# Kernel tuning notes

Measured on AMD Instinct MI355X. Metric: run time of the kernel, lower is better.

Reference implementation:

```python
import jax, jax.numpy as jnp
import numpy as np

B, N, H, E = 1, 50000, 8, 32
P = 1_600_000  # num edges


def setup_inputs() -> dict:
    key = jax.random.key(0)
    kq, kk, kv, ka = jax.random.split(key, 4)
    queries = jax.random.normal(kq, (B, N, H, E), dtype=jnp.float32)
    keys = jax.random.normal(kk, (B, N, H, E), dtype=jnp.float32)
    values = jax.random.normal(kv, (B, N, H, E), dtype=jnp.float32)
    adj = jax.random.randint(ka, (2, P), 0, N, dtype=jnp.int32)
    return {"queries": queries, "keys": keys, "values": values, "adj": adj}


def reference(queries, keys, values, adj):
    # queries/keys: (B, N, H, E); values: (B, N, H, D); adj: (2, P) COO edges
    b, n, h, e = queries.shape
    temp = 1.0 / np.sqrt(e).astype(np.float32)
    src, dst = adj[0], adj[1]
    # per-edge scaled dot product: (P, B, H), edge axis leading for segment ops
    s = temp * jnp.einsum("bphe,bphe->pbh", queries[:, src], keys[:, dst])
    # segment (scatter) softmax keyed by target node src
    m = jax.ops.segment_max(s, src, num_segments=n)          # (N, B, H)
    p = jnp.exp(s - m[src])                                   # (P, B, H)
    den = jax.ops.segment_sum(p, src, num_segments=n)        # (N, B, H)
    alpha = p / den[src]                                      # (P, B, H)
    # sparse weighted aggregation (spmm): out[i] = sum_{e: src==i} alpha_e * v[dst_e]
    vg = jnp.moveaxis(values[:, dst], 0, 1)                   # (P, B, H, D)
    out = jax.ops.segment_sum(alpha[..., None] * vg, src, num_segments=n)  # (N, B, H, D)
    return jnp.moveaxis(out, 0, 1)                            # (B, N, H, D)
```

## Files before the change

### kernel.cpp

```cpp
#include <hip/hip_runtime.h>
#include <hip/hip_fp16.h>
#include <math.h>

#define HEADS 8
#define EDIM 32
#define ROW (HEADS * EDIM)

typedef _Float16 h2_t __attribute__((ext_vector_type(2)));

__device__ __forceinline__ void pack_one(const float* __restrict__ k, const float* __restrict__ v,
                                         uint4* __restrict__ kvh, long t) {
    const float4 kf = *reinterpret_cast<const float4*>(k + t * 4);
    const float4 vf = *reinterpret_cast<const float4*>(v + t * 4);
    __half2 h0 = __floats2half2_rn(kf.x, kf.y);
    __half2 h1 = __floats2half2_rn(kf.z, kf.w);
    __half2 h2 = __floats2half2_rn(vf.x, vf.y);
    __half2 h3 = __floats2half2_rn(vf.z, vf.w);
    uint4 o;
    o.x = *reinterpret_cast<unsigned int*>(&h0);
    o.y = *reinterpret_cast<unsigned int*>(&h1);
    o.z = *reinterpret_cast<unsigned int*>(&h2);
    o.w = *reinterpret_cast<unsigned int*>(&h3);
    kvh[t] = o;
}

__global__ __launch_bounds__(256) void prep_fused_kernel(
    const float* __restrict__ k, const float* __restrict__ v, uint4* __restrict__ kvh,
    const int* __restrict__ src, const int* __restrict__ dst,
    int* __restrict__ counts, int* __restrict__ padded,
    int N, int P, int scatBlocks, int cap, int copies)
{
    if ((int)blockIdx.x < scatBlocks) {
        const int copy = (int)blockIdx.x & (copies - 1);
        int* __restrict__ cnt = counts + (size_t)copy * N;
        int* __restrict__ pad = padded + (size_t)copy * N * cap;
        const int P2 = P >> 1;
        const int stride = scatBlocks * 256;
        int i = (int)blockIdx.x * 256 + threadIdx.x;
        for (; i < P2; i += stride) {
            const int2 s2 = reinterpret_cast<const int2*>(src)[i];
            const int2 d2 = reinterpret_cast<const int2*>(dst)[i];
            int pos = atomicAdd(&cnt[s2.x], 1);
            if (pos < cap) pad[(size_t)s2.x * cap + pos] = d2.x;
            pos = atomicAdd(&cnt[s2.y], 1);
            if (pos < cap) pad[(size_t)s2.y * cap + pos] = d2.y;
        }
        if ((P & 1) && blockIdx.x == 0 && threadIdx.x == 0) {
            const int s = src[P - 1];
            const int pos = atomicAdd(&cnt[s], 1);
            if (pos < cap) pad[(size_t)s * cap + pos] = dst[P - 1];
        }
    } else {
        const long t = (long)((int)blockIdx.x - scatBlocks) * 256 + threadIdx.x;
        if (t < (long)N * 64) pack_one(k, v, kvh, t);
    }
}

__global__ __launch_bounds__(256) void pack_kernel(const float* __restrict__ k,
                                                   const float* __restrict__ v,
                                                   uint4* __restrict__ kvh, long total) {
    const long t = (long)blockIdx.x * blockDim.x + threadIdx.x;
    if (t < total) pack_one(k, v, kvh, t);
}

__global__ void hist_kernel(const int* __restrict__ src, int* __restrict__ counts, int P) {
    int i = blockIdx.x * blockDim.x + threadIdx.x;
    int stride = gridDim.x * blockDim.x;
    for (; i < P; i += stride) atomicAdd(&counts[src[i]], 1);
}

__global__ __launch_bounds__(1024) void scan_block(const int* __restrict__ counts,
                                                   int* __restrict__ loc_excl,
                                                   int* __restrict__ bsums, int n) {
    __shared__ int wsum[16];
    const int lane = threadIdx.x & 63;
    const int wv = threadIdx.x >> 6;
    const int i = blockIdx.x * 1024 + threadIdx.x;
    const int val = (i < n) ? counts[i] : 0;
    int incl = val;
    #pragma unroll
    for (int off = 1; off < 64; off <<= 1) {
        int t = __shfl_up(incl, off);
        if (lane >= off) incl += t;
    }
    if (lane == 63) wsum[wv] = incl;
    __syncthreads();
    if (threadIdx.x < 16) {
        int wval = wsum[threadIdx.x];
        int winc = wval;
        #pragma unroll
        for (int off = 1; off < 16; off <<= 1) {
            int t = __shfl_up(winc, off);
            if ((int)threadIdx.x >= off) winc += t;
        }
        wsum[threadIdx.x] = winc - wval;
    }
    __syncthreads();
    const int ex = wsum[wv] + incl - val;
    if (i < n) loc_excl[i] = ex;
    if (threadIdx.x == 1023) bsums[blockIdx.x] = ex + val;
}

__global__ void scan_tops(const int* __restrict__ bsums, int* __restrict__ bbase,
                          int nb, int* __restrict__ total_out) {
    const int lane = threadIdx.x & 63;
    int base = 0;
    for (int start = 0; start < nb; start += 64) {
        const int idx = start + lane;
        const int v = (idx < nb) ? bsums[idx] : 0;
        int incl = v;
        #pragma unroll
        for (int off = 1; off < 64; off <<= 1) {
            int t = __shfl_up(incl, off);
            if (lane >= off) incl += t;
        }
        if (idx < nb) bbase[idx] = base + incl - v;
        base += __shfl(incl, 63);
    }
    if (lane == 0) *total_out = base;
}

__global__ void scan_add(const int* __restrict__ loc_excl, const int* __restrict__ bbase,
                         int* __restrict__ offsets, int* __restrict__ cursors, int n) {
    const int i = blockIdx.x * blockDim.x + threadIdx.x;
    if (i < n) {
        const int o = loc_excl[i] + bbase[i >> 10];
        offsets[i] = o;
        cursors[i] = o;
    }
}

__global__ void scatter_kernel(const int* __restrict__ src, const int* __restrict__ dst,
                               int* __restrict__ cursors, int* __restrict__ sorted_dst, int P) {
    int i = blockIdx.x * blockDim.x + threadIdx.x;
    int stride = gridDim.x * blockDim.x;
    for (; i < P; i += stride) {
        int s = src[i];
        int pos = atomicAdd(&cursors[s], 1);
        sorted_dst[pos] = dst[i];
    }
}

__device__ __forceinline__ void edge_accum(const uint4 raw, const h2_t qh01, const h2_t qh23,
                                           float& lsum, float4& acc) {
    const h2_t k01 = *reinterpret_cast<const h2_t*>(&raw.x);
    const h2_t k23 = *reinterpret_cast<const h2_t*>(&raw.y);
    const float2 v01 = __half22float2(*reinterpret_cast<const __half2*>(&raw.z));
    const float2 v23 = __half22float2(*reinterpret_cast<const __half2*>(&raw.w));
    float p = __builtin_amdgcn_fdot2(qh01, k01,
              __builtin_amdgcn_fdot2(qh23, k23, 0.0f, false), false);
    p += __shfl_xor(p, 1);
    p += __shfl_xor(p, 2);
    p += __shfl_xor(p, 4);
    const float w = __expf(p);
    lsum += w;
    acc.x += w * v01.x; acc.y += w * v01.y;
    acc.z += w * v23.x; acc.w += w * v23.y;
}

__global__ __launch_bounds__(256) void attn_kernel_h(
    const float* __restrict__ q, const uint4* __restrict__ kv,
    const int* __restrict__ counts_or_offsets, const int* __restrict__ edges,
    float* __restrict__ out, int N, float temp, int cap, int copies)
{
    const int wave = threadIdx.x >> 6;
    const int lane = threadIdx.x & 63;
    const int node = blockIdx.x * 4 + wave;
    if (node >= N) return;

    float4 qv = *reinterpret_cast<const float4*>(q + (size_t)node * ROW + lane * 4);
    qv.x *= temp; qv.y *= temp; qv.z *= temp; qv.w *= temp;
    const __half2 qp01 = __floats2half2_rn(qv.x, qv.y);
    const __half2 qp23 = __floats2half2_rn(qv.z, qv.w);
    const h2_t qh01 = *reinterpret_cast<const h2_t*>(&qp01);
    const h2_t qh23 = *reinterpret_cast<const h2_t*>(&qp23);
    const uint4* kvl = kv + lane;

    float lsum = 0.0f;
    float4 acc = {0.f, 0.f, 0.f, 0.f};

    if (cap > 0) {
        for (int c = 0; c < copies; ++c) {
            int cnt = counts_or_offsets[(size_t)c * N + node];
            cnt = (cnt < cap) ? cnt : cap;
            const int* __restrict__ bucket = edges + ((size_t)c * N + node) * cap;
            int i = 0;
            for (; i + 2 <= cnt; i += 2) {
                const int d0 = bucket[i];
                const int d1 = bucket[i + 1];
                const uint4 r0 = kvl[(size_t)d0 * 64];
                const uint4 r1 = kvl[(size_t)d1 * 64];
                edge_accum(r0, qh01, qh23, lsum, acc);
                edge_accum(r1, qh01, qh23, lsum, acc);
            }
            if (i < cnt) {
                const uint4 r = kvl[(size_t)bucket[i] * 64];
                edge_accum(r, qh01, qh23, lsum, acc);
            }
        }
    } else {
        int e = counts_or_offsets[node];
        const int end = counts_or_offsets[node + 1];
        for (; e + 2 <= end; e += 2) {
            const int d0 = edges[e];
            const int d1 = edges[e + 1];
            const uint4 r0 = kvl[(size_t)d0 * 64];
            const uint4 r1 = kvl[(size_t)d1 * 64];
            edge_accum(r0, qh01, qh23, lsum, acc);
            edge_accum(r1, qh01, qh23, lsum, acc);
        }
        if (e < end) {
            const uint4 r = kvl[(size_t)edges[e] * 64];
            edge_accum(r, qh01, qh23, lsum, acc);
        }
    }

    const float inv = (lsum > 0.0f) ? (1.0f / lsum) : 0.0f;
    float4 o;
    o.x = acc.x * inv; o.y = acc.y * inv; o.z = acc.z * inv; o.w = acc.w * inv;
    *reinterpret_cast<float4*>(out + (size_t)node * ROW + lane * 4) = o;
}

extern "C" void kernel_launch(void* const* d_in, const int* in_sizes, int n_in,
                              void* d_out, int out_size, void* d_ws, size_t ws_size,
                              hipStream_t stream) {
    const float* q = (const float*)d_in[0];
    const float* k = (const float*)d_in[1];
    const float* v = (const float*)d_in[2];
    const int*   adj = (const int*)d_in[3];

    const int N = in_sizes[0] / ROW;
    const int P = in_sizes[3] / 2;
    const int* src = adj;
    const int* dst = adj + P;

    const float temp = 1.0f / sqrtf((float)EDIM);
    const size_t kv_bytes = (size_t)N * 64 * sizeof(uint4);

    const int tier_copies[3] = {8, 4, 1};
    const int tier_cap[3]    = {20, 28, 96};

    for (int t = 0; t < 3; ++t) {
        const int copies = tier_copies[t];
        const int cap = tier_cap[t];
        const size_t int_bytes = (size_t)copies * N * (1 + cap) * sizeof(int);
        const size_t kv_off = (int_bytes + 15) & ~(size_t)15;
        if (ws_size < kv_off + kv_bytes) continue;

        int* counts = (int*)d_ws;
        int* padded = counts + (size_t)copies * N;
        uint4* kvh = (uint4*)((char*)d_ws + kv_off);

        hipMemsetAsync(counts, 0, (size_t)copies * N * sizeof(int), stream);

        const int packBlocks = (int)(((long)N * 64 + 255) / 256);
        const int scatBlocks = 3072;
        prep_fused_kernel<<<scatBlocks + packBlocks, 256, 0, stream>>>(
            k, v, kvh, src, dst, counts, padded, N, P, scatBlocks, cap, copies);

        attn_kernel_h<<<(N + 3) / 4, 256, 0, stream>>>(q, kvh, counts, padded,
                                                       (float*)d_out, N, temp, cap, copies);
        return;
    }

    const int nb = (N + 1023) / 1024;
    int* counts  = (int*)d_ws;
    int* offsets = counts + N;
    int* cursors = offsets + N + 1;
    int* sorted  = cursors + N;
    int* bsums   = sorted + P;
    int* bbase   = bsums + nb;
    size_t int_bytes = (size_t)(3 * N + 1 + P + 2 * nb) * sizeof(int);
    size_t kv_off = (int_bytes + 15) & ~(size_t)15;
    uint4* kvh = (uint4*)((char*)d_ws + kv_off);

    hipMemsetAsync(counts, 0, (size_t)N * sizeof(int), stream);
    pack_kernel<<<(int)(((long)N * 64 + 255) / 256), 256, 0, stream>>>(k, v, kvh, (long)N * 64);
    hist_kernel<<<2048, 256, 0, stream>>>(src, counts, P);
    scan_block<<<nb, 1024, 0, stream>>>(counts, counts, bsums, N);
    scan_tops<<<1, 64, 0, stream>>>(bsums, bbase, nb, offsets + N);
    scan_add<<<(N + 255) / 256, 256, 0, stream>>>(counts, bbase, offsets, cursors, N);
    scatter_kernel<<<2048, 256, 0, stream>>>(src, dst, cursors, sorted, P);
    attn_kernel_h<<<(N + 3) / 4, 256, 0, stream>>>(q, kvh, offsets, sorted,
                                                   (float*)d_out, N, temp, 0, 1);
}
```

Baseline: 378.3 us.

## Interleave scatter and pack blocks in fused prep kernel, add nontemporal streaming

Scatter blocks are now interleaved with pack blocks (one of every 13 blocks does scatter), so atomic-heavy bucket building runs concurrently with bandwidth-bound K/V fp16 packing instead of the scatter blocks all being scheduled first. The scatter loop is restructured to issue four independent loads and atomics per iteration to raise memory-level parallelism. Streaming inputs and outputs (K/V, q, out, packed kv) use nontemporal loads and stores to avoid polluting cache. The scatter block count changes (about 1042 instead of 3072), which lowers scatter parallelism, and nontemporal stores of kvh may hurt reuse in the following attention kernel.

```diff
diff --git a/kernel.cpp b/kernel.cpp
--- a/kernel.cpp
+++ b/kernel.cpp
@@ -5,60 +5,75 @@
 #define HEADS 8
 #define EDIM 32
 #define ROW (HEADS * EDIM)
+#define ILV 13
 
 typedef _Float16 h2_t __attribute__((ext_vector_type(2)));
+typedef float f4v __attribute__((ext_vector_type(4)));
+typedef unsigned int u4v __attribute__((ext_vector_type(4)));
 
 __device__ __forceinline__ void pack_one(const float* __restrict__ k, const float* __restrict__ v,
-                                         uint4* __restrict__ kvh, long t) {
-    const float4 kf = *reinterpret_cast<const float4*>(k + t * 4);
-    const float4 vf = *reinterpret_cast<const float4*>(v + t * 4);
+                                         unsigned int* __restrict__ kvh, long t) {
+    const f4v kf = __builtin_nontemporal_load(reinterpret_cast<const f4v*>(k) + t);
+    const f4v vf = __builtin_nontemporal_load(reinterpret_cast<const f4v*>(v) + t);
     __half2 h0 = __floats2half2_rn(kf.x, kf.y);
     __half2 h1 = __floats2half2_rn(kf.z, kf.w);
     __half2 h2 = __floats2half2_rn(vf.x, vf.y);
     __half2 h3 = __floats2half2_rn(vf.z, vf.w);
-    uint4 o;
+    u4v o;
     o.x = *reinterpret_cast<unsigned int*>(&h0);
     o.y = *reinterpret_cast<unsigned int*>(&h1);
     o.z = *reinterpret_cast<unsigned int*>(&h2);
     o.w = *reinterpret_cast<unsigned int*>(&h3);
-    kvh[t] = o;
+    __builtin_nontemporal_store(o, reinterpret_cast<u4v*>(kvh) + t);
 }
 
 __global__ __launch_bounds__(256) void prep_fused_kernel(
-    const float* __restrict__ k, const float* __restrict__ v, uint4* __restrict__ kvh,
+    const float* __restrict__ k, const float* __restrict__ v, unsigned int* __restrict__ kvh,
     const int* __restrict__ src, const int* __restrict__ dst,
     int* __restrict__ counts, int* __restrict__ padded,
     int N, int P, int scatBlocks, int cap, int copies)
 {
-    if ((int)blockIdx.x < scatBlocks) {
-        const int copy = (int)blockIdx.x & (copies - 1);
+    const int g = (int)blockIdx.x;
+    const int s = g / ILV;
+    const int r = g - s * ILV;
+    if (r == ILV - 1) {
+        const int copy = g & (copies - 1);
         int* __restrict__ cnt = counts + (size_t)copy * N;
         int* __restrict__ pad = padded + (size_t)copy * N * cap;
-        const int P2 = P >> 1;
         const int stride = scatBlocks * 256;
-        int i = (int)blockIdx.x * 256 + threadIdx.x;
-        for (; i < P2; i += stride) {
-            const int2 s2 = reinterpret_cast<const int2*>(src)[i];
-            const int2 d2 = reinterpret_cast<const int2*>(dst)[i];
-            int pos = atomicAdd(&cnt[s2.x], 1);
-            if (pos < cap) pad[(size_t)s2.x * cap + pos] = d2.x;
-            pos = atomicAdd(&cnt[s2.y], 1);
-            if (pos < cap) pad[(size_t)s2.y * cap + pos] = d2.y;
-        }
-        if ((P & 1) && blockIdx.x == 0 && threadIdx.x == 0) {
-            const int s = src[P - 1];
-            const int pos = atomicAdd(&cnt[s], 1);
-            if (pos < cap) pad[(size_t)s * cap + pos] = dst[P - 1];
+        int i = s * 256 + (int)threadIdx.x;
+        for (; i + 3 * stride < P; i += 4 * stride) {
+            const int s0 = src[i];
+            const int s1 = src[i + stride];
+            const int s2 = src[i + 2 * stride];
+            const int s3 = src[i + 3 * stride];
+            const int d0 = dst[i];
+            const int d1 = dst[i + stride];
+            const int d2 = dst[i + 2 * stride];
+            const int d3 = dst[i + 3 * stride];
+            const int p0 = atomicAdd(&cnt[s0], 1);
+            const int p1 = atomicAdd(&cnt[s1], 1);
+            const int p2 = atomicAdd(&cnt[s2], 1);
+            const int p3 = atomicAdd(&cnt[s3], 1);
+            if (p0 < cap) pad[(size_t)s0 * cap + p0] = d0;
+            if (p1 < cap) pad[(size_t)s1 * cap + p1] = d1;
+            if (p2 < cap) pad[(size_t)s2 * cap + p2] = d2;
+            if (p3 < cap) pad[(size_t)s3 * cap + p3] = d3;
+        }
+        for (; i < P; i += stride) {
+            const int sv = src[i];
+            const int pos = atomicAdd(&cnt[sv], 1);
+            if (pos < cap) pad[(size_t)sv * cap + pos] = dst[i];
         }
     } else {
-        const long t = (long)((int)blockIdx.x - scatBlocks) * 256 + threadIdx.x;
+        const long t = (long)(s * (ILV - 1) + r) * 256 + threadIdx.x;
         if (t < (long)N * 64) pack_one(k, v, kvh, t);
     }
 }
 
 __global__ __launch_bounds__(256) void pack_kernel(const float* __restrict__ k,
                                                    const float* __restrict__ v,
-                                                   uint4* __restrict__ kvh, long total) {
+                                                   unsigned int* __restrict__ kvh, long total) {
     const long t = (long)blockIdx.x * blockDim.x + threadIdx.x;
     if (t < total) pack_one(k, v, kvh, t);
 }
@@ -168,7 +183,8 @@
     const int node = blockIdx.x * 4 + wave;
     if (node >= N) return;
 
-    float4 qv = *reinterpret_cast<const float4*>(q + (size_t)node * ROW + lane * 4);
+    f4v qv = __builtin_nontemporal_load(
+        reinterpret_cast<const f4v*>(q + (size_t)node * ROW) + lane);
     qv.x *= temp; qv.y *= temp; qv.z *= temp; qv.w *= temp;
     const __half2 qp01 = __floats2half2_rn(qv.x, qv.y);
     const __half2 qp23 = __floats2half2_rn(qv.z, qv.w);
@@ -216,9 +232,9 @@
     }
 
     const float inv = (lsum > 0.0f) ? (1.0f / lsum) : 0.0f;
-    float4 o;
+    f4v o;
     o.x = acc.x * inv; o.y = acc.y * inv; o.z = acc.z * inv; o.w = acc.w * inv;
-    *reinterpret_cast<float4*>(out + (size_t)node * ROW + lane * 4) = o;
+    __builtin_nontemporal_store(o, reinterpret_cast<f4v*>(out + (size_t)node * ROW) + lane);
 }
 
 extern "C" void kernel_launch(void* const* d_in, const int* in_sizes, int n_in,
@@ -249,16 +265,16 @@
 
         int* counts = (int*)d_ws;
         int* padded = counts + (size_t)copies * N;
-        uint4* kvh = (uint4*)((char*)d_ws + kv_off);
+        unsigned int* kvh = (unsigned int*)((char*)d_ws + kv_off);
 
         hipMemsetAsync(counts, 0, (size_t)copies * N * sizeof(int), stream);
 
         const int packBlocks = (int)(((long)N * 64 + 255) / 256);
-        const int scatBlocks = 3072;
-        prep_fused_kernel<<<scatBlocks + packBlocks, 256, 0, stream>>>(
+        const int scatBlocks = (packBlocks + ILV - 2) / (ILV - 1);
+        prep_fused_kernel<<<scatBlocks * ILV, 256, 0, stream>>>(
             k, v, kvh, src, dst, counts, padded, N, P, scatBlocks, cap, copies);
 
-        attn_kernel_h<<<(N + 3) / 4, 256, 0, stream>>>(q, kvh, counts, padded,
+        attn_kernel_h<<<(N + 3) / 4, 256, 0, stream>>>(q, (const uint4*)kvh, counts, padded,
                                                        (float*)d_out, N, temp, cap, copies);
         return;
     }
@@ -272,7 +288,7 @@
     int* bbase   = bsums + nb;
     size_t int_bytes = (size_t)(3 * N + 1 + P + 2 * nb) * sizeof(int);
     size_t kv_off = (int_bytes + 15) & ~(size_t)15;
-    uint4* kvh = (uint4*)((char*)d_ws + kv_off);
+    unsigned int* kvh = (unsigned int*)((char*)d_ws + kv_off);
 
     hipMemsetAsync(counts, 0, (size_t)N * sizeof(int), stream);
     pack_kernel<<<(int)(((long)N * 64 + 255) / 256), 256, 0, stream>>>(k, v, kvh, (long)N * 64);
@@ -281,6 +297,6 @@
     scan_tops<<<1, 64, 0, stream>>>(bsums, bbase, nb, offsets + N);
     scan_add<<<(N + 255) / 256, 256, 0, stream>>>(counts, bbase, offsets, cursors, N);
     scatter_kernel<<<2048, 256, 0, stream>>>(src, dst, cursors, sorted, P);
-    attn_kernel_h<<<(N + 3) / 4, 256, 0, stream>>>(q, kvh, offsets, sorted,
+    attn_kernel_h<<<(N + 3) / 4, 256, 0, stream>>>(q, (const uint4*)kvh, offsets, sorted,
                                                    (float*)d_out, N, temp, 0, 1);
 }
```

New measurement: 322.4 us. 1.17x faster.
